# Performance work log

Hardware: AMD Instinct MI355X
Metric: run time of the kernel (lower is better)

Reference implementation:

```python
import jax, jax.numpy as jnp
import numpy as np

E = 1408      # hidden_size
H = 16        # num heads
D = E // H    # head_dim = 88
S = 1025      # (448/14)^2 + 1 cls token
B = 8


def setup_inputs() -> dict:
    key = jax.random.key(0)
    ks = jax.random.split(key, 11)
    scale = 1.0 / np.sqrt(E)
    inp = {
        "hidden_states": jax.random.normal(ks[0], (B, S, E), dtype=jnp.float32),
    }
    # rotary freqs as cos/sin of random angles, shape (S, D//2)
    theta = jax.random.uniform(ks[1], (S, D // 2), dtype=jnp.float32) * (2.0 * np.pi)
    inp["freqs_cos"] = jnp.cos(theta)
    inp["freqs_sin"] = jnp.sin(theta)
    # projection weights stored torch-style: (out_features, in_features)
    inp["q_w"] = jax.random.normal(ks[2], (E, E), dtype=jnp.float32) * scale
    inp["q_b"] = jax.random.normal(ks[3], (E,), dtype=jnp.float32) * scale
    inp["k_w"] = jax.random.normal(ks[4], (E, E), dtype=jnp.float32) * scale
    inp["k_b"] = jax.random.normal(ks[5], (E,), dtype=jnp.float32) * scale
    inp["v_w"] = jax.random.normal(ks[6], (E, E), dtype=jnp.float32) * scale
    inp["v_b"] = jax.random.normal(ks[7], (E,), dtype=jnp.float32) * scale
    inp["o_w"] = jax.random.normal(ks[8], (E, E), dtype=jnp.float32) * scale
    inp["o_b"] = jax.random.normal(ks[9], (E,), dtype=jnp.float32) * scale
    return inp


def _apply_rope(x, cos, sin):
    # x: (B, S, H, D); interpret last dim as D//2 complex pairs (re, im)
    xr = x.astype(jnp.float32).reshape(*x.shape[:-1], D // 2, 2)
    re, im = xr[..., 0], xr[..., 1]
    c = cos[None, :, None, :]  # broadcast over batch and heads
    s = sin[None, :, None, :]
    out_re = re * c - im * s
    out_im = re * s + im * c
    return jnp.stack([out_re, out_im], axis=-1).reshape(x.shape).astype(x.dtype)


def reference(hidden_states, freqs_cos, freqs_sin, q_w, q_b, k_w, k_b, v_w, v_b, o_w, o_b):
    b, s, _ = hidden_states.shape
    q = (hidden_states @ q_w.T + q_b).reshape(b, s, H, D)
    k = (hidden_states @ k_w.T + k_b).reshape(b, s, H, D)
    v = (hidden_states @ v_w.T + v_b).reshape(b, s, H, D)
    q = _apply_rope(q, freqs_cos, freqs_sin)
    k = _apply_rope(k, freqs_cos, freqs_sin)
    # (B, H, S, D)
    q = q.transpose(0, 2, 1, 3)
    k = k.transpose(0, 2, 1, 3)
    v = v.transpose(0, 2, 1, 3)
    scores = jnp.einsum('bhqd,bhkd->bhqk', q, k) / np.sqrt(D)
    attn = jax.nn.softmax(scores.astype(jnp.float32), axis=-1).astype(q.dtype)
    out = jnp.einsum('bhqk,bhkd->bqhd', attn, v).reshape(b, s, H * D)
    out = out @ o_w.T + o_b
    return out, attn
```

## Files before the change

### kernel.cpp

```cpp
#include <hip/hip_runtime.h>

typedef unsigned short u16;
typedef __attribute__((ext_vector_type(8))) short short8;
typedef __attribute__((ext_vector_type(4))) float f32x4;
typedef __attribute__((ext_vector_type(16))) float f32x16;

#define E_DIM 1408
#define H_HEADS 16
#define S_SEQ 1025
#define B_BATCH 8
#define S_PAD 1088
#define D_PAD 128
#define M_ROWS 8200
#define M_PAD 8320

struct __attribute__((packed, aligned(4))) f4u { float x, y, z, w; };

__device__ __forceinline__ u16 f2bf(float f){
  union { float f; unsigned u; } x; x.f = f;
  unsigned r = x.u + 0x7fffu + ((x.u >> 16) & 1u);
  return (u16)(r >> 16);
}

__device__ __forceinline__ void gload16(const void* g, void* l){
  __builtin_amdgcn_global_load_lds(
      (const __attribute__((address_space(1))) void*)g,
      (__attribute__((address_space(3))) void*)l, 16, 0, 0);
}

__device__ __forceinline__ f32x4 mfma16(short8 a, short8 b, f32x4 c){
  return __builtin_amdgcn_mfma_f32_16x16x32_bf16(a, b, c, 0, 0, 0);
}
__device__ __forceinline__ f32x16 mfma32(short8 a, short8 b, f32x16 c){
  return __builtin_amdgcn_mfma_f32_32x32x16_bf16(a, b, c, 0, 0, 0);
}

__device__ __forceinline__ unsigned cvtpk(float a, float b){
  unsigned r;
  asm("v_cvt_pk_bf16_f32 %0, %1, %2" : "=v"(r) : "v"(a), "v"(b));
  return r;
}
__device__ __forceinline__ void plswap(unsigned &a, unsigned &b){
  asm("v_permlane32_swap_b32 %0, %1" : "+v"(a), "+v"(b));
}

__global__ __launch_bounds__(256) void cvt_kernel(const float* __restrict__ src,
                                                  u16* __restrict__ dst, int n8){
  int i = blockIdx.x * 256 + threadIdx.x;
  if (i >= n8) return;
  const float4* s4 = (const float4*)src;
  float4 a = s4[2*i], b = s4[2*i+1];
  union { u16 u[8]; short8 v; } o;
  o.u[0]=f2bf(a.x); o.u[1]=f2bf(a.y); o.u[2]=f2bf(a.z); o.u[3]=f2bf(a.w);
  o.u[4]=f2bf(b.x); o.u[5]=f2bf(b.y); o.u[6]=f2bf(b.z); o.u[7]=f2bf(b.w);
  ((short8*)dst)[i] = o.v;
}

__global__ __launch_bounds__(256) void cvt4_kernel(const float* __restrict__ s0,
                                                   const float* __restrict__ s1,
                                                   const float* __restrict__ s2,
                                                   const float* __restrict__ s3,
                                                   u16* __restrict__ dst, int n8){
  int i = blockIdx.x * 256 + threadIdx.x;
  if (i >= n8) return;
  const float* src = (blockIdx.y == 0) ? s0 : (blockIdx.y == 1) ? s1
                   : (blockIdx.y == 2) ? s2 : s3;
  u16* d = dst + (size_t)blockIdx.y * n8 * 8;
  const float4* s4 = (const float4*)src;
  float4 a = s4[2*i], b = s4[2*i+1];
  union { u16 u[8]; short8 v; } o;
  o.u[0]=f2bf(a.x); o.u[1]=f2bf(a.y); o.u[2]=f2bf(a.z); o.u[3]=f2bf(a.w);
  o.u[4]=f2bf(b.x); o.u[5]=f2bf(b.y); o.u[6]=f2bf(b.z); o.u[7]=f2bf(b.w);
  ((short8*)d)[i] = o.v;
}

__global__ __launch_bounds__(256) void zero_pads_kernel(u16* __restrict__ Q,
                                                        u16* __restrict__ K,
                                                        u16* __restrict__ Vt){
  int i = blockIdx.x * 256 + threadIdx.x;
  const int n1 = 128 * S_PAD * 8;
  const int n2 = 128 * 63 * 96;
  const int n3 = 128 * 96 * 63;
  if (i < n1){
    int d = 88 + (i & 7); int t = i >> 3;
    int s = t % S_PAD; int bh = t / S_PAD;
    size_t o = ((size_t)bh * S_PAD + s) * D_PAD + d;
    Q[o] = 0; K[o] = 0;
  } else if (i < n1 + n2){
    int j = i - n1;
    int d = j % 96; int t = j / 96;
    int s = 1025 + t % 63; int bh = t / 63;
    size_t o = ((size_t)bh * S_PAD + s) * D_PAD + d;
    Q[o] = 0; K[o] = 0;
  } else if (i < n1 + n2 + n3){
    int j = i - n1 - n2;
    int d = j % 96; int t = j / 96;
    int sp = 1025 + t % 63; int bh = t / 63;
    Vt[((size_t)bh * D_PAD + d) * S_PAD + sp] = 0;
  }
}

template<int MODE>
__global__ __launch_bounds__(256) void gemm_bt(
    const u16* __restrict__ A, const u16* __restrict__ W,
    const float* __restrict__ b_q, const float* __restrict__ b_k,
    const float* __restrict__ b_v,
    u16* __restrict__ Qb, u16* __restrict__ Kb, u16* __restrict__ Vtb,
    float* __restrict__ outF,
    const float* __restrict__ fcos, const float* __restrict__ fsin)
{
  __shared__ u16 As[128*32];
  __shared__ u16 Bs[128*32];
  const int tid = threadIdx.x;
  const int lane = tid & 63, wid = tid >> 6;
  const int cl = lane & 15, grp = lane >> 4;

  const int nwg = (int)(gridDim.x * gridDim.y);
  const int orig = blockIdx.x + gridDim.x * blockIdx.y;
  const int qq = nwg >> 3, rr = nwg & 7;
  const int xcd = orig & 7, kk = orig >> 3;
  const int wg = (xcd < rr ? xcd * (qq + 1) : rr * (qq + 1) + (xcd - rr) * qq) + kk;
  const int bx = wg % (int)gridDim.x, by = wg / (int)gridDim.x;

  const int n0 = bx * 128, m0 = by * 128;
  const int region = (MODE == 0) ? (bx / 11) : 0;
  const int wm = (wid >> 1) * 64, wn = (wid & 1) * 64;
  f32x4 acc[4][4] = {};

  for (int k0 = 0; k0 < E_DIM; k0 += 32){
    __syncthreads();
#pragma unroll
    for (int rd = 0; rd < 2; ++rd){
      int G = rd * 256 + tid;
      int row = G >> 2, cg = G & 3;
      gload16(A + (size_t)(m0 + row) * E_DIM + k0 + cg * 8, (char*)As + (size_t)G * 16);
      gload16(W + (size_t)(n0 + row) * E_DIM + k0 + cg * 8, (char*)Bs + (size_t)G * 16);
    }
    __syncthreads();
    short8 av[4], bv[4];
#pragma unroll
    for (int i = 0; i < 4; ++i) av[i] = *(const short8*)&As[(wm + i*16 + cl)*32 + grp*8];
#pragma unroll
    for (int j = 0; j < 4; ++j) bv[j] = *(const short8*)&Bs[(wn + j*16 + cl)*32 + grp*8];
    __builtin_amdgcn_s_setprio(1);
#pragma unroll
    for (int i = 0; i < 4; ++i)
#pragma unroll
      for (int j = 0; j < 4; ++j)
        acc[i][j] = mfma16(av[i], bv[j], acc[i][j]);
    __builtin_amdgcn_s_setprio(0);
  }

  const float* bias = (MODE == 1) ? b_q : (region == 0 ? b_q : (region == 1 ? b_k : b_v));
  const float QSCALE = 0.15379181f;

#pragma unroll
  for (int i = 0; i < 4; ++i){
#pragma unroll
    for (int j = 0; j < 4; ++j){
      const int jcol = n0 + wn + j*16 + cl;
      const int jl = jcol - region * E_DIM;
      const float bsv = bias[jl];
      const int hh = jl / 88;
      const int dd = jl - hh * 88;
#pragma unroll
      for (int r = 0; r < 4; ++r){
        const int rrow = m0 + wm + i*16 + grp*4 + r;
        float v = acc[i][j][r] + bsv;
        if (MODE == 0 && region <= 1){
          float other = __shfl_xor(v, 1);
          int bb = rrow / 1025;
          int spos = rrow - bb * 1025;
          int pp = dd >> 1;
          float c = fcos[spos * 44 + pp];
          float s = fsin[spos * 44 + pp];
          float o = fmaf(v, c, (jl & 1) ? (other * s) : -(other * s));
          if (region == 0) o *= QSCALE;
          if (rrow < M_ROWS){
            size_t dst = (((size_t)(bb * 16 + hh)) * S_PAD + spos) * D_PAD + dd;
            (region ? Kb : Qb)[dst] = f2bf(o);
          }
        } else if (MODE == 0){
          if (rrow < M_ROWS){
            int bb = rrow / 1025;
            int spos = rrow - bb * 1025;
            size_t dst = (((size_t)(bb * 16 + hh)) * D_PAD + dd) * S_PAD + spos;
            Vtb[dst] = f2bf(v);
          }
        } else {
          if (rrow < M_ROWS) outF[(size_t)rrow * E_DIM + jcol] = v;
        }
      }
    }
  }
}

#define STAGE_K(buf, kt)                                                        \
  {                                                                             \
    _Pragma("unroll")                                                           \
    for (int rd = 0; rd < 4; ++rd){                                             \
      int G = rd * 256 + tid;                                                   \
      int row = G >> 4, c = G & 15;                                             \
      gload16(Kg + (size_t)((kt) * 64 + row) * 128 + ((c ^ (row & 15)) * 8),    \
              (char*)&Ks[buf][0] + (size_t)G * 16);                             \
    }                                                                           \
  }

#define STAGE_V(kt)                                                             \
  {                                                                             \
    _Pragma("unroll")                                                           \
    for (int rd = 0; rd < 3; ++rd){                                             \
      int G = rd * 256 + tid;                                                   \
      int row = G >> 3, c = G & 7;                                              \
      gload16(Vg + (size_t)row * S_PAD + (kt) * 64 + ((c ^ (row & 7)) * 8),     \
              (char*)Vs + (size_t)G * 16);                                      \
    }                                                                           \
  }

__global__ __launch_bounds__(256, 3) void attn_kernel(
    const u16* __restrict__ Qb, const u16* __restrict__ Kb,
    const u16* __restrict__ Vtb, float* __restrict__ attn,
    u16* __restrict__ AO)
{
  __shared__ u16 Ks[2][64 * 128];
  __shared__ u16 Vs[96 * 64];
  const int tid = threadIdx.x, wid = tid >> 6, lane = tid & 63;
  const int q5 = lane & 31, hi = lane >> 5;
  int lin = blockIdx.x + gridDim.x * blockIdx.y;
  lin = (lin & 7) * 144 + (lin >> 3);
  const int qt = lin % 9, bh = lin / 9;
  const int b = bh >> 4, h = bh & 15;
  const u16* __restrict__ Qg = Qb + (size_t)bh * S_PAD * 128;
  const u16* __restrict__ Kg = Kb + (size_t)bh * S_PAD * 128;
  const u16* __restrict__ Vg = Vtb + (size_t)bh * 128 * S_PAD;
  const int qrow = qt * 128 + wid * 32 + q5;
  const int qrowc = (qrow < S_PAD) ? qrow : (S_PAD - 1);

  short8 qf[6];
#pragma unroll
  for (int ds = 0; ds < 6; ++ds)
    qf[ds] = *(const short8*)&Qg[(size_t)qrowc * 128 + ds * 16 + hi * 8];

  float l0 = 0.f, l1 = 0.f, l2 = 0.f, l3 = 0.f;
  STAGE_K(0, 0);
  __syncthreads();
  for (int kt = 0; kt < 17; ++kt){
    const int cur = kt & 1;
    if (kt < 16) STAGE_K(cur ^ 1, kt + 1);
#pragma unroll
    for (int ks = 0; ks < 2; ++ks){
      f32x16 sc = {};
      const int krow = ks * 32 + q5;
      __builtin_amdgcn_s_setprio(1);
#pragma unroll
      for (int ds = 0; ds < 6; ++ds){
        int c = ds * 2 + hi;
        short8 kf = *(const short8*)&Ks[cur][krow * 128 + ((c ^ (krow & 15)) * 8)];
        sc = mfma32(kf, qf[ds], sc);
      }
      __builtin_amdgcn_s_setprio(0);
#pragma unroll
      for (int r = 0; r < 16; r += 4){
        l0 += __builtin_amdgcn_exp2f(sc[r]);
        l1 += __builtin_amdgcn_exp2f(sc[r+1]);
        l2 += __builtin_amdgcn_exp2f(sc[r+2]);
        l3 += __builtin_amdgcn_exp2f(sc[r+3]);
      }
    }
    __syncthreads();
  }
  float l = (l0 + l1) + (l2 + l3);
  l += __shfl_xor(l, 32);
  l -= 63.0f;
  const float lg2l = __builtin_amdgcn_logf(l);

  f32x16 oacc[3] = {};
  STAGE_K(0, 0);
  STAGE_V(0);
  __syncthreads();
  for (int kt = 0; kt < 17; ++kt){
    const int cur = kt & 1;
    if (kt < 16) STAGE_K(cur ^ 1, kt + 1);
    short8 pa0[2], pa1[2];
#pragma unroll
    for (int ks = 0; ks < 2; ++ks){
      f32x16 sc = {};
      const int krow = ks * 32 + q5;
      __builtin_amdgcn_s_setprio(1);
#pragma unroll
      for (int ds = 0; ds < 6; ++ds){
        int c = ds * 2 + hi;
        short8 kf = *(const short8*)&Ks[cur][krow * 128 + ((c ^ (krow & 15)) * 8)];
        sc = mfma32(kf, qf[ds], sc);
      }
      __builtin_amdgcn_s_setprio(0);
#pragma unroll
      for (int r = 0; r < 16; ++r) sc[r] = __builtin_amdgcn_exp2f(sc[r] - lg2l);

      if (qrow < 1025){
        if (kt < 16){
          float* arow = attn + ((size_t)bh * 1025 + qrow) * 1025 + kt * 64 + ks * 32 + 4 * hi;
#pragma unroll
          for (int g = 0; g < 4; ++g){
            f4u w4 = { sc[4*g], sc[4*g+1], sc[4*g+2], sc[4*g+3] };
            *(f4u*)(arow + 8 * g) = w4;
          }
        } else {
#pragma unroll
          for (int r = 0; r < 16; ++r){
            int kabs = 1024 + ks * 32 + (r & 3) + 8 * (r >> 2) + 4 * hi;
            if (kabs < 1025)
              attn[((size_t)bh * 1025 + qrow) * 1025 + kabs] = sc[r];
          }
        }
      }

      unsigned w0 = cvtpk(sc[0],  sc[1]),  w1 = cvtpk(sc[2],  sc[3]);
      unsigned w2 = cvtpk(sc[4],  sc[5]),  w3 = cvtpk(sc[6],  sc[7]);
      unsigned w4 = cvtpk(sc[8],  sc[9]),  w5 = cvtpk(sc[10], sc[11]);
      unsigned w6 = cvtpk(sc[12], sc[13]), w7 = cvtpk(sc[14], sc[15]);
      plswap(w0, w2); plswap(w1, w3); plswap(w4, w6); plswap(w5, w7);
      union U { unsigned u[4]; short8 s8; } A0, A1;
      A0.u[0] = w0; A0.u[1] = w1; A0.u[2] = w2; A0.u[3] = w3;
      A1.u[0] = w4; A1.u[1] = w5; A1.u[2] = w6; A1.u[3] = w7;
      pa0[ks] = A0.s8; pa1[ks] = A1.s8;
    }

    __syncthreads();
    __builtin_amdgcn_s_setprio(1);
#pragma unroll
    for (int ks = 0; ks < 2; ++ks){
#pragma unroll
      for (int dt = 0; dt < 3; ++dt){
        const int vrow = dt * 32 + q5;
        int c0 = ks * 4 + hi;
        short8 vf0 = *(const short8*)&Vs[vrow * 64 + ((c0 ^ (vrow & 7)) * 8)];
        oacc[dt] = mfma32(pa0[ks], vf0, oacc[dt]);
        int c1 = ks * 4 + 2 + hi;
        short8 vf1 = *(const short8*)&Vs[vrow * 64 + ((c1 ^ (vrow & 7)) * 8)];
        oacc[dt] = mfma32(pa1[ks], vf1, oacc[dt]);
      }
    }
    __builtin_amdgcn_s_setprio(0);
    __syncthreads();
    if (kt < 16) STAGE_V(kt + 1);
  }

  const int qb0 = qt * 128 + wid * 32;
#pragma unroll
  for (int dt = 0; dt < 3; ++dt){
    const int d = dt * 32 + q5;
    if (d < 88){
#pragma unroll
      for (int r = 0; r < 16; ++r){
        int qq2 = qb0 + (r & 3) + 8 * (r >> 2) + 4 * hi;
        if (qq2 < 1025)
          AO[((size_t)b * 1025 + qq2) * E_DIM + h * 88 + d] = f2bf(oacc[dt][r]);
      }
    }
  }
}

extern "C" void kernel_launch(void* const* d_in, const int* in_sizes, int n_in,
                              void* d_out, int out_size, void* d_ws, size_t ws_size,
                              hipStream_t stream)
{
  const float* hs   = (const float*)d_in[0];
  const float* fcos = (const float*)d_in[1];
  const float* fsin = (const float*)d_in[2];
  const float* q_w  = (const float*)d_in[3];
  const float* q_b  = (const float*)d_in[4];
  const float* k_w  = (const float*)d_in[5];
  const float* k_b  = (const float*)d_in[6];
  const float* v_w  = (const float*)d_in[7];
  const float* v_b  = (const float*)d_in[8];
  const float* o_w  = (const float*)d_in[9];
  const float* o_b  = (const float*)d_in[10];
  float* out0 = (float*)d_out;
  float* attn = out0 + (size_t)B_BATCH * S_SEQ * E_DIM;

  char* ws = (char*)d_ws;
  size_t off = 0;
  auto take = [&](size_t bytes){
    char* p = ws + off; off += (bytes + 255) & ~(size_t)255; return p;
  };
  u16* Xb  = (u16*)take((size_t)M_PAD * E_DIM * 2);
  u16* Wb  = (u16*)take((size_t)4 * E_DIM * E_DIM * 2);
  u16* Qb  = (u16*)take((size_t)128 * S_PAD * D_PAD * 2);
  u16* Kb  = (u16*)take((size_t)128 * S_PAD * D_PAD * 2);
  u16* Vtb = (u16*)take((size_t)128 * D_PAD * S_PAD * 2);
  u16* AO  = (u16*)take((size_t)M_PAD * E_DIM * 2);

  cvt_kernel<<<(1443200 + 255) / 256, 256, 0, stream>>>(hs, Xb, 1443200);
  cvt4_kernel<<<dim3(968, 4), 256, 0, stream>>>(q_w, k_w, v_w, o_w, Wb, 247808);
  zero_pads_kernel<<<10400, 256, 0, stream>>>(Qb, Kb, Vtb);

  gemm_bt<0><<<dim3(33, 65), 256, 0, stream>>>(Xb, Wb, q_b, k_b, v_b,
                                               Qb, Kb, Vtb, nullptr, fcos, fsin);

  attn_kernel<<<dim3(9, 128), 256, 0, stream>>>(Qb, Kb, Vtb, attn, AO);

  gemm_bt<1><<<dim3(11, 65), 256, 0, stream>>>(AO, Wb + 3 * (size_t)E_DIM * E_DIM,
                                               o_b, o_b, o_b,
                                               nullptr, nullptr, nullptr, out0, fcos, fsin);
}
```

Baseline: 547.9 us.

## Use 256x256 double-buffered swizzled tile GEMM for fused QKV projection

Replaces the 128x128 single-buffered QKV GEMM with a 512-thread kernel using 256x256 tiles, K-step 64 split into two halves, double-buffered LDS with async global-to-LDS loads, and an XOR swizzle to cut bank conflicts. Weight buffer is padded to 4352 rows and X to 8448 rows so the larger tiles fit, with masks on the epilogue writes. The output projection moves into its own unchanged-style kernel. The larger tiles and overlapped loads are meant to raise data reuse and hide memory latency. In exchange, LDS and register use per block rise, the padded columns cost wasted MFMA work, and the padded rows/weights are read uninitialized.

```diff
diff --git a/kernel.cpp b/kernel.cpp
--- a/kernel.cpp
+++ b/kernel.cpp
@@ -12,7 +12,9 @@
 #define S_PAD 1088
 #define D_PAD 128
 #define M_ROWS 8200
-#define M_PAD 8320
+#define M_PAD 8448
+#define N_QKV 4224
+#define N_QKV_PAD 4352
 
 struct __attribute__((packed, aligned(4))) f4u { float x, y, z, w; };
 
@@ -56,15 +58,13 @@
   ((short8*)dst)[i] = o.v;
 }
 
-__global__ __launch_bounds__(256) void cvt4_kernel(const float* __restrict__ s0,
+__global__ __launch_bounds__(256) void cvt3_kernel(const float* __restrict__ s0,
                                                    const float* __restrict__ s1,
                                                    const float* __restrict__ s2,
-                                                   const float* __restrict__ s3,
                                                    u16* __restrict__ dst, int n8){
   int i = blockIdx.x * 256 + threadIdx.x;
   if (i >= n8) return;
-  const float* src = (blockIdx.y == 0) ? s0 : (blockIdx.y == 1) ? s1
-                   : (blockIdx.y == 2) ? s2 : s3;
+  const float* src = (blockIdx.y == 0) ? s0 : (blockIdx.y == 1) ? s1 : s2;
   u16* d = dst + (size_t)blockIdx.y * n8 * 8;
   const float4* s4 = (const float4*)src;
   float4 a = s4[2*i], b = s4[2*i+1];
@@ -100,74 +100,105 @@
   }
 }
 
-template<int MODE>
-__global__ __launch_bounds__(256) void gemm_bt(
-    const u16* __restrict__ A, const u16* __restrict__ W,
+#define STG(buf, mat, h, t)                                                     \
+  {                                                                             \
+    const u16* gsrc = (mat) ? (Wq + (size_t)n0 * E_DIM) : (Aq + (size_t)m0 * E_DIM); \
+    _Pragma("unroll")                                                           \
+    for (int rd = 0; rd < 2; ++rd){                                             \
+      int L = rd * 512 + tid;                                                   \
+      int r = L >> 2;                                                           \
+      int g = (L & 3) ^ ((r >> 1) & 3);                                         \
+      gload16(gsrc + (size_t)r * E_DIM + (t) * 64 + (h) * 32 + g * 8,           \
+              (char*)&Ls[buf][mat][h][0] + (size_t)L * 16);                     \
+    }                                                                           \
+  }
+
+#define COMPUTE(buf, ks)                                                        \
+  {                                                                             \
+    short8 av[8], bv[4];                                                        \
+    _Pragma("unroll")                                                           \
+    for (int i = 0; i < 8; ++i){                                                \
+      int R = wm + i * 16 + cl;                                                 \
+      av[i] = *(const short8*)&Ls[buf][0][ks][R * 32 + ((grp ^ ((R >> 1) & 3)) * 8)]; \
+    }                                                                           \
+    _Pragma("unroll")                                                           \
+    for (int j = 0; j < 4; ++j){                                                \
+      int R = wn + j * 16 + cl;                                                 \
+      bv[j] = *(const short8*)&Ls[buf][1][ks][R * 32 + ((grp ^ ((R >> 1) & 3)) * 8)]; \
+    }                                                                           \
+    __builtin_amdgcn_s_setprio(1);                                              \
+    _Pragma("unroll")                                                           \
+    for (int i = 0; i < 8; ++i)                                                 \
+      _Pragma("unroll")                                                         \
+      for (int j = 0; j < 4; ++j)                                               \
+        acc[i][j] = mfma16(av[i], bv[j], acc[i][j]);                            \
+    __builtin_amdgcn_s_setprio(0);                                              \
+  }
+
+#define WAITV(n) asm volatile("s_waitcnt vmcnt(" #n ")" ::: "memory")
+
+__global__ __launch_bounds__(512, 2) void gemm_qkv256(
+    const u16* __restrict__ Aq, const u16* __restrict__ Wq,
     const float* __restrict__ b_q, const float* __restrict__ b_k,
     const float* __restrict__ b_v,
     u16* __restrict__ Qb, u16* __restrict__ Kb, u16* __restrict__ Vtb,
-    float* __restrict__ outF,
     const float* __restrict__ fcos, const float* __restrict__ fsin)
 {
-  __shared__ u16 As[128*32];
-  __shared__ u16 Bs[128*32];
+  __shared__ u16 Ls[2][2][2][256 * 32];
   const int tid = threadIdx.x;
   const int lane = tid & 63, wid = tid >> 6;
   const int cl = lane & 15, grp = lane >> 4;
 
-  const int nwg = (int)(gridDim.x * gridDim.y);
+  const int nwg = 17 * 33;
   const int orig = blockIdx.x + gridDim.x * blockIdx.y;
   const int qq = nwg >> 3, rr = nwg & 7;
   const int xcd = orig & 7, kk = orig >> 3;
   const int wg = (xcd < rr ? xcd * (qq + 1) : rr * (qq + 1) + (xcd - rr) * qq) + kk;
-  const int bx = wg % (int)gridDim.x, by = wg / (int)gridDim.x;
-
-  const int n0 = bx * 128, m0 = by * 128;
-  const int region = (MODE == 0) ? (bx / 11) : 0;
-  const int wm = (wid >> 1) * 64, wn = (wid & 1) * 64;
-  f32x4 acc[4][4] = {};
-
-  for (int k0 = 0; k0 < E_DIM; k0 += 32){
-    __syncthreads();
-#pragma unroll
-    for (int rd = 0; rd < 2; ++rd){
-      int G = rd * 256 + tid;
-      int row = G >> 2, cg = G & 3;
-      gload16(A + (size_t)(m0 + row) * E_DIM + k0 + cg * 8, (char*)As + (size_t)G * 16);
-      gload16(W + (size_t)(n0 + row) * E_DIM + k0 + cg * 8, (char*)Bs + (size_t)G * 16);
-    }
-    __syncthreads();
-    short8 av[4], bv[4];
-#pragma unroll
-    for (int i = 0; i < 4; ++i) av[i] = *(const short8*)&As[(wm + i*16 + cl)*32 + grp*8];
-#pragma unroll
-    for (int j = 0; j < 4; ++j) bv[j] = *(const short8*)&Bs[(wn + j*16 + cl)*32 + grp*8];
-    __builtin_amdgcn_s_setprio(1);
-#pragma unroll
-    for (int i = 0; i < 4; ++i)
-#pragma unroll
-      for (int j = 0; j < 4; ++j)
-        acc[i][j] = mfma16(av[i], bv[j], acc[i][j]);
-    __builtin_amdgcn_s_setprio(0);
-  }
-
-  const float* bias = (MODE == 1) ? b_q : (region == 0 ? b_q : (region == 1 ? b_k : b_v));
+  const int bx = wg % 17, by = wg / 17;
+  const int n0 = bx * 256, m0 = by * 256;
+  const int wm = (wid >> 2) * 128, wn = (wid & 3) * 64;
+
+  f32x4 acc[8][4] = {};
+
+  STG(0, 0, 0, 0); STG(0, 1, 0, 0);
+  STG(0, 0, 1, 0); STG(0, 1, 1, 0);
+
+  for (int kt = 0; kt < 21; ++kt){
+    const int cur = kt & 1, nxt = cur ^ 1;
+    WAITV(4);
+    __builtin_amdgcn_s_barrier();
+    STG(nxt, 0, 0, kt + 1); STG(nxt, 1, 0, kt + 1);
+    COMPUTE(cur, 0);
+    WAITV(4);
+    __builtin_amdgcn_s_barrier();
+    STG(nxt, 0, 1, kt + 1); STG(nxt, 1, 1, kt + 1);
+    COMPUTE(cur, 1);
+  }
+  WAITV(4);
+  __builtin_amdgcn_s_barrier();
+  COMPUTE(1, 0);
+  WAITV(0);
+  __builtin_amdgcn_s_barrier();
+  COMPUTE(1, 1);
+
   const float QSCALE = 0.15379181f;
-
-#pragma unroll
-  for (int i = 0; i < 4; ++i){
-#pragma unroll
-    for (int j = 0; j < 4; ++j){
-      const int jcol = n0 + wn + j*16 + cl;
-      const int jl = jcol - region * E_DIM;
-      const float bsv = bias[jl];
-      const int hh = jl / 88;
-      const int dd = jl - hh * 88;
+#pragma unroll
+  for (int j = 0; j < 4; ++j){
+    const int jcol = n0 + wn + j * 16 + cl;
+    const bool vcol = (jcol < N_QKV);
+    const int region = vcol ? (jcol / E_DIM) : 2;
+    const int jl = jcol - region * E_DIM;
+    const float* bias = (region == 0) ? b_q : (region == 1) ? b_k : b_v;
+    const float bsv = vcol ? bias[jl] : 0.f;
+    const int hh = jl / 88;
+    const int dd = jl - hh * 88;
+#pragma unroll
+    for (int i = 0; i < 8; ++i){
 #pragma unroll
       for (int r = 0; r < 4; ++r){
-        const int rrow = m0 + wm + i*16 + grp*4 + r;
+        const int rrow = m0 + wm + i * 16 + grp * 4 + r;
         float v = acc[i][j][r] + bsv;
-        if (MODE == 0 && region <= 1){
+        if (region <= 1){
           float other = __shfl_xor(v, 1);
           int bb = rrow / 1025;
           int spos = rrow - bb * 1025;
@@ -176,20 +207,78 @@
           float s = fsin[spos * 44 + pp];
           float o = fmaf(v, c, (jl & 1) ? (other * s) : -(other * s));
           if (region == 0) o *= QSCALE;
-          if (rrow < M_ROWS){
+          if (vcol && rrow < M_ROWS && dd < 88){
             size_t dst = (((size_t)(bb * 16 + hh)) * S_PAD + spos) * D_PAD + dd;
             (region ? Kb : Qb)[dst] = f2bf(o);
           }
-        } else if (MODE == 0){
-          if (rrow < M_ROWS){
+        } else {
+          if (vcol && rrow < M_ROWS && dd < 88){
             int bb = rrow / 1025;
             int spos = rrow - bb * 1025;
             size_t dst = (((size_t)(bb * 16 + hh)) * D_PAD + dd) * S_PAD + spos;
             Vtb[dst] = f2bf(v);
           }
-        } else {
-          if (rrow < M_ROWS) outF[(size_t)rrow * E_DIM + jcol] = v;
         }
+      }
+    }
+  }
+}
+
+__global__ __launch_bounds__(256) void gemm_oproj(
+    const u16* __restrict__ A, const u16* __restrict__ W,
+    const float* __restrict__ bias, float* __restrict__ outF)
+{
+  __shared__ u16 As[128*32];
+  __shared__ u16 Bs[128*32];
+  const int tid = threadIdx.x;
+  const int lane = tid & 63, wid = tid >> 6;
+  const int cl = lane & 15, grp = lane >> 4;
+
+  const int nwg = (int)(gridDim.x * gridDim.y);
+  const int orig = blockIdx.x + gridDim.x * blockIdx.y;
+  const int qq = nwg >> 3, rr = nwg & 7;
+  const int xcd = orig & 7, kk = orig >> 3;
+  const int wg = (xcd < rr ? xcd * (qq + 1) : rr * (qq + 1) + (xcd - rr) * qq) + kk;
+  const int bx = wg % (int)gridDim.x, by = wg / (int)gridDim.x;
+
+  const int n0 = bx * 128, m0 = by * 128;
+  const int wm = (wid >> 1) * 64, wn = (wid & 1) * 64;
+  f32x4 acc[4][4] = {};
+
+  for (int k0 = 0; k0 < E_DIM; k0 += 32){
+    __syncthreads();
+#pragma unroll
+    for (int rd = 0; rd < 2; ++rd){
+      int G = rd * 256 + tid;
+      int row = G >> 2, cg = G & 3;
+      gload16(A + (size_t)(m0 + row) * E_DIM + k0 + cg * 8, (char*)As + (size_t)G * 16);
+      gload16(W + (size_t)(n0 + row) * E_DIM + k0 + cg * 8, (char*)Bs + (size_t)G * 16);
+    }
+    __syncthreads();
+    short8 av[4], bv[4];
+#pragma unroll
+    for (int i = 0; i < 4; ++i) av[i] = *(const short8*)&As[(wm + i*16 + cl)*32 + grp*8];
+#pragma unroll
+    for (int j = 0; j < 4; ++j) bv[j] = *(const short8*)&Bs[(wn + j*16 + cl)*32 + grp*8];
+    __builtin_amdgcn_s_setprio(1);
+#pragma unroll
+    for (int i = 0; i < 4; ++i)
+#pragma unroll
+      for (int j = 0; j < 4; ++j)
+        acc[i][j] = mfma16(av[i], bv[j], acc[i][j]);
+    __builtin_amdgcn_s_setprio(0);
+  }
+
+#pragma unroll
+  for (int i = 0; i < 4; ++i){
+#pragma unroll
+    for (int j = 0; j < 4; ++j){
+      const int jcol = n0 + wn + j*16 + cl;
+      const float bsv = bias[jcol];
+#pragma unroll
+      for (int r = 0; r < 4; ++r){
+        const int rrow = m0 + wm + i*16 + grp*4 + r;
+        if (rrow < M_ROWS) outF[(size_t)rrow * E_DIM + jcol] = acc[i][j][r] + bsv;
       }
     }
   }
@@ -384,23 +473,23 @@
   auto take = [&](size_t bytes){
     char* p = ws + off; off += (bytes + 255) & ~(size_t)255; return p;
   };
-  u16* Xb  = (u16*)take((size_t)M_PAD * E_DIM * 2);
-  u16* Wb  = (u16*)take((size_t)4 * E_DIM * E_DIM * 2);
-  u16* Qb  = (u16*)take((size_t)128 * S_PAD * D_PAD * 2);
-  u16* Kb  = (u16*)take((size_t)128 * S_PAD * D_PAD * 2);
-  u16* Vtb = (u16*)take((size_t)128 * D_PAD * S_PAD * 2);
-  u16* AO  = (u16*)take((size_t)M_PAD * E_DIM * 2);
+  u16* Xb   = (u16*)take((size_t)M_PAD * E_DIM * 2);
+  u16* Wqkv = (u16*)take((size_t)N_QKV_PAD * E_DIM * 2);
+  u16* Wo   = (u16*)take((size_t)E_DIM * E_DIM * 2);
+  u16* Qb   = (u16*)take((size_t)128 * S_PAD * D_PAD * 2);
+  u16* Kb   = (u16*)take((size_t)128 * S_PAD * D_PAD * 2);
+  u16* Vtb  = (u16*)take((size_t)128 * D_PAD * S_PAD * 2);
+  u16* AO   = (u16*)take((size_t)M_PAD * E_DIM * 2);
 
   cvt_kernel<<<(1443200 + 255) / 256, 256, 0, stream>>>(hs, Xb, 1443200);
-  cvt4_kernel<<<dim3(968, 4), 256, 0, stream>>>(q_w, k_w, v_w, o_w, Wb, 247808);
+  cvt3_kernel<<<dim3(968, 3), 256, 0, stream>>>(q_w, k_w, v_w, Wqkv, 247808);
+  cvt_kernel<<<968, 256, 0, stream>>>(o_w, Wo, 247808);
   zero_pads_kernel<<<10400, 256, 0, stream>>>(Qb, Kb, Vtb);
 
-  gemm_bt<0><<<dim3(33, 65), 256, 0, stream>>>(Xb, Wb, q_b, k_b, v_b,
-                                               Qb, Kb, Vtb, nullptr, fcos, fsin);
+  gemm_qkv256<<<dim3(17, 33), 512, 0, stream>>>(Xb, Wqkv, q_b, k_b, v_b,
+                                                Qb, Kb, Vtb, fcos, fsin);
 
   attn_kernel<<<dim3(9, 128), 256, 0, stream>>>(Qb, Kb, Vtb, attn, AO);
 
-  gemm_bt<1><<<dim3(11, 65), 256, 0, stream>>>(AO, Wb + 3 * (size_t)E_DIM * E_DIM,
-                                               o_b, o_b, o_b,
-                                               nullptr, nullptr, nullptr, out0, fcos, fsin);
-}
+  gemm_oproj<<<dim3(11, 65), 256, 0, stream>>>(AO, Wo, o_b, out0);
+}
```

Measured after the change: 580.6 us. 1.06x slower.

## Split attention into two kernels and read K/V directly from global memory

Applied to the files above, without the earlier changes.

The fused attention kernel becomes two kernels. The first computes the per-row softmax log-normaliser and stores it to a workspace buffer. The second recomputes the scores, writes the normalised attention and accumulates P·V. Both now load K and V fragments straight from global memory instead of staging them through LDS with barriers, which frees shared memory and removes syncthreads, and pass 1 may run at higher occupancy. The risk is redundant global traffic from uncoalesced, unshared K/V loads, plus an extra launch. Weight conversion is also split into separate QKV and output buffers.

```diff
diff --git a/kernel.cpp b/kernel.cpp
--- a/kernel.cpp
+++ b/kernel.cpp
@@ -13,6 +13,7 @@
 #define D_PAD 128
 #define M_ROWS 8200
 #define M_PAD 8320
+#define N_QKV 4224
 
 struct __attribute__((packed, aligned(4))) f4u { float x, y, z, w; };
 
@@ -56,15 +57,13 @@
   ((short8*)dst)[i] = o.v;
 }
 
-__global__ __launch_bounds__(256) void cvt4_kernel(const float* __restrict__ s0,
+__global__ __launch_bounds__(256) void cvt3_kernel(const float* __restrict__ s0,
                                                    const float* __restrict__ s1,
                                                    const float* __restrict__ s2,
-                                                   const float* __restrict__ s3,
                                                    u16* __restrict__ dst, int n8){
   int i = blockIdx.x * 256 + threadIdx.x;
   if (i >= n8) return;
-  const float* src = (blockIdx.y == 0) ? s0 : (blockIdx.y == 1) ? s1
-                   : (blockIdx.y == 2) ? s2 : s3;
+  const float* src = (blockIdx.y == 0) ? s0 : (blockIdx.y == 1) ? s1 : s2;
   u16* d = dst + (size_t)blockIdx.y * n8 * 8;
   const float4* s4 = (const float4*)src;
   float4 a = s4[2*i], b = s4[2*i+1];
@@ -195,35 +194,61 @@
   }
 }
 
-#define STAGE_K(buf, kt)                                                        \
-  {                                                                             \
-    _Pragma("unroll")                                                           \
-    for (int rd = 0; rd < 4; ++rd){                                             \
-      int G = rd * 256 + tid;                                                   \
-      int row = G >> 4, c = G & 15;                                             \
-      gload16(Kg + (size_t)((kt) * 64 + row) * 128 + ((c ^ (row & 15)) * 8),    \
-              (char*)&Ks[buf][0] + (size_t)G * 16);                             \
-    }                                                                           \
-  }
-
-#define STAGE_V(kt)                                                             \
-  {                                                                             \
-    _Pragma("unroll")                                                           \
-    for (int rd = 0; rd < 3; ++rd){                                             \
-      int G = rd * 256 + tid;                                                   \
-      int row = G >> 3, c = G & 7;                                              \
-      gload16(Vg + (size_t)row * S_PAD + (kt) * 64 + ((c ^ (row & 7)) * 8),     \
-              (char*)Vs + (size_t)G * 16);                                      \
-    }                                                                           \
-  }
-
-__global__ __launch_bounds__(256, 3) void attn_kernel(
+
+__global__ __launch_bounds__(256, 4) void attn_pass1(
     const u16* __restrict__ Qb, const u16* __restrict__ Kb,
-    const u16* __restrict__ Vtb, float* __restrict__ attn,
-    u16* __restrict__ AO)
+    float* __restrict__ lw)
 {
-  __shared__ u16 Ks[2][64 * 128];
-  __shared__ u16 Vs[96 * 64];
+  const int tid = threadIdx.x, wid = tid >> 6, lane = tid & 63;
+  const int q5 = lane & 31, hi = lane >> 5;
+  int lin = blockIdx.x + gridDim.x * blockIdx.y;
+  lin = (lin & 7) * 144 + (lin >> 3);
+  const int qt = lin % 9, bh = lin / 9;
+  const u16* __restrict__ Qg = Qb + (size_t)bh * S_PAD * 128;
+  const u16* __restrict__ Kg = Kb + (size_t)bh * S_PAD * 128;
+  const int qrow = qt * 128 + wid * 32 + q5;
+  const int qrowc = (qrow < S_PAD) ? qrow : (S_PAD - 1);
+
+  short8 qf[6];
+#pragma unroll
+  for (int ds = 0; ds < 6; ++ds)
+    qf[ds] = *(const short8*)&Qg[(size_t)qrowc * 128 + ds * 16 + hi * 8];
+
+  float l0 = 0.f, l1 = 0.f, l2 = 0.f, l3 = 0.f;
+  for (int kt = 0; kt < 17; ++kt){
+#pragma unroll
+    for (int ks = 0; ks < 2; ++ks){
+      const int krow = kt * 64 + ks * 32 + q5;
+      short8 kf[6];
+#pragma unroll
+      for (int ds = 0; ds < 6; ++ds)
+        kf[ds] = *(const short8*)&Kg[(size_t)krow * 128 + (ds * 2 + hi) * 8];
+      f32x16 sc = {};
+      __builtin_amdgcn_s_setprio(1);
+#pragma unroll
+      for (int ds = 0; ds < 6; ++ds) sc = mfma32(kf[ds], qf[ds], sc);
+      __builtin_amdgcn_s_setprio(0);
+#pragma unroll
+      for (int r = 0; r < 16; r += 4){
+        l0 += __builtin_amdgcn_exp2f(sc[r]);
+        l1 += __builtin_amdgcn_exp2f(sc[r+1]);
+        l2 += __builtin_amdgcn_exp2f(sc[r+2]);
+        l3 += __builtin_amdgcn_exp2f(sc[r+3]);
+      }
+    }
+  }
+  float l = (l0 + l1) + (l2 + l3);
+  l += __shfl_xor(l, 32);
+  l -= 63.0f;
+  if (hi == 0 && qrow < S_PAD)
+    lw[(size_t)bh * S_PAD + qrow] = __builtin_amdgcn_logf(l);
+}
+
+__global__ __launch_bounds__(256, 3) void attn_pass2(
+    const u16* __restrict__ Qb, const u16* __restrict__ Kb,
+    const u16* __restrict__ Vtb, const float* __restrict__ lw,
+    float* __restrict__ attn, u16* __restrict__ AO)
+{
   const int tid = threadIdx.x, wid = tid >> 6, lane = tid & 63;
   const int q5 = lane & 31, hi = lane >> 5;
   int lin = blockIdx.x + gridDim.x * blockIdx.y;
@@ -240,62 +265,25 @@
 #pragma unroll
   for (int ds = 0; ds < 6; ++ds)
     qf[ds] = *(const short8*)&Qg[(size_t)qrowc * 128 + ds * 16 + hi * 8];
-
-  float l0 = 0.f, l1 = 0.f, l2 = 0.f, l3 = 0.f;
-  STAGE_K(0, 0);
-  __syncthreads();
+  const float lgl = lw[(size_t)bh * S_PAD + qrowc];
+
+  f32x16 oacc[3] = {};
   for (int kt = 0; kt < 17; ++kt){
-    const int cur = kt & 1;
-    if (kt < 16) STAGE_K(cur ^ 1, kt + 1);
+    short8 pa0[2], pa1[2];
 #pragma unroll
     for (int ks = 0; ks < 2; ++ks){
+      const int krow = kt * 64 + ks * 32 + q5;
+      short8 kf[6];
+#pragma unroll
+      for (int ds = 0; ds < 6; ++ds)
+        kf[ds] = *(const short8*)&Kg[(size_t)krow * 128 + (ds * 2 + hi) * 8];
       f32x16 sc = {};
-      const int krow = ks * 32 + q5;
       __builtin_amdgcn_s_setprio(1);
 #pragma unroll
-      for (int ds = 0; ds < 6; ++ds){
-        int c = ds * 2 + hi;
-        short8 kf = *(const short8*)&Ks[cur][krow * 128 + ((c ^ (krow & 15)) * 8)];
-        sc = mfma32(kf, qf[ds], sc);
-      }
+      for (int ds = 0; ds < 6; ++ds) sc = mfma32(kf[ds], qf[ds], sc);
       __builtin_amdgcn_s_setprio(0);
 #pragma unroll
-      for (int r = 0; r < 16; r += 4){
-        l0 += __builtin_amdgcn_exp2f(sc[r]);
-        l1 += __builtin_amdgcn_exp2f(sc[r+1]);
-        l2 += __builtin_amdgcn_exp2f(sc[r+2]);
-        l3 += __builtin_amdgcn_exp2f(sc[r+3]);
-      }
-    }
-    __syncthreads();
-  }
-  float l = (l0 + l1) + (l2 + l3);
-  l += __shfl_xor(l, 32);
-  l -= 63.0f;
-  const float lg2l = __builtin_amdgcn_logf(l);
-
-  f32x16 oacc[3] = {};
-  STAGE_K(0, 0);
-  STAGE_V(0);
-  __syncthreads();
-  for (int kt = 0; kt < 17; ++kt){
-    const int cur = kt & 1;
-    if (kt < 16) STAGE_K(cur ^ 1, kt + 1);
-    short8 pa0[2], pa1[2];
-#pragma unroll
-    for (int ks = 0; ks < 2; ++ks){
-      f32x16 sc = {};
-      const int krow = ks * 32 + q5;
-      __builtin_amdgcn_s_setprio(1);
-#pragma unroll
-      for (int ds = 0; ds < 6; ++ds){
-        int c = ds * 2 + hi;
-        short8 kf = *(const short8*)&Ks[cur][krow * 128 + ((c ^ (krow & 15)) * 8)];
-        sc = mfma32(kf, qf[ds], sc);
-      }
-      __builtin_amdgcn_s_setprio(0);
-#pragma unroll
-      for (int r = 0; r < 16; ++r) sc[r] = __builtin_amdgcn_exp2f(sc[r] - lg2l);
+      for (int r = 0; r < 16; ++r) sc[r] = __builtin_amdgcn_exp2f(sc[r] - lgl);
 
       if (qrow < 1025){
         if (kt < 16){
@@ -326,24 +314,19 @@
       pa0[ks] = A0.s8; pa1[ks] = A1.s8;
     }
 
-    __syncthreads();
     __builtin_amdgcn_s_setprio(1);
 #pragma unroll
     for (int ks = 0; ks < 2; ++ks){
 #pragma unroll
       for (int dt = 0; dt < 3; ++dt){
         const int vrow = dt * 32 + q5;
-        int c0 = ks * 4 + hi;
-        short8 vf0 = *(const short8*)&Vs[vrow * 64 + ((c0 ^ (vrow & 7)) * 8)];
+        short8 vf0 = *(const short8*)&Vg[(size_t)vrow * S_PAD + kt * 64 + (ks * 4 + hi) * 8];
         oacc[dt] = mfma32(pa0[ks], vf0, oacc[dt]);
-        int c1 = ks * 4 + 2 + hi;
-        short8 vf1 = *(const short8*)&Vs[vrow * 64 + ((c1 ^ (vrow & 7)) * 8)];
+        short8 vf1 = *(const short8*)&Vg[(size_t)vrow * S_PAD + kt * 64 + (ks * 4 + 2 + hi) * 8];
         oacc[dt] = mfma32(pa1[ks], vf1, oacc[dt]);
       }
     }
     __builtin_amdgcn_s_setprio(0);
-    __syncthreads();
-    if (kt < 16) STAGE_V(kt + 1);
   }
 
   const int qb0 = qt * 128 + wid * 32;
@@ -384,23 +367,26 @@
   auto take = [&](size_t bytes){
     char* p = ws + off; off += (bytes + 255) & ~(size_t)255; return p;
   };
-  u16* Xb  = (u16*)take((size_t)M_PAD * E_DIM * 2);
-  u16* Wb  = (u16*)take((size_t)4 * E_DIM * E_DIM * 2);
-  u16* Qb  = (u16*)take((size_t)128 * S_PAD * D_PAD * 2);
-  u16* Kb  = (u16*)take((size_t)128 * S_PAD * D_PAD * 2);
-  u16* Vtb = (u16*)take((size_t)128 * D_PAD * S_PAD * 2);
-  u16* AO  = (u16*)take((size_t)M_PAD * E_DIM * 2);
+  u16* Xb   = (u16*)take((size_t)M_PAD * E_DIM * 2);
+  u16* Wqkv = (u16*)take((size_t)N_QKV * E_DIM * 2);
+  u16* Wo   = (u16*)take((size_t)E_DIM * E_DIM * 2);
+  u16* Qb   = (u16*)take((size_t)128 * S_PAD * D_PAD * 2);
+  u16* Kb   = (u16*)take((size_t)128 * S_PAD * D_PAD * 2);
+  u16* Vtb  = (u16*)take((size_t)128 * D_PAD * S_PAD * 2);
+  u16* AO   = (u16*)take((size_t)M_PAD * E_DIM * 2);
+  float* lw = (float*)take((size_t)128 * S_PAD * 4);
 
   cvt_kernel<<<(1443200 + 255) / 256, 256, 0, stream>>>(hs, Xb, 1443200);
-  cvt4_kernel<<<dim3(968, 4), 256, 0, stream>>>(q_w, k_w, v_w, o_w, Wb, 247808);
+  cvt3_kernel<<<dim3(968, 3), 256, 0, stream>>>(q_w, k_w, v_w, Wqkv, 247808);
+  cvt_kernel<<<968, 256, 0, stream>>>(o_w, Wo, 247808);
   zero_pads_kernel<<<10400, 256, 0, stream>>>(Qb, Kb, Vtb);
 
-  gemm_bt<0><<<dim3(33, 65), 256, 0, stream>>>(Xb, Wb, q_b, k_b, v_b,
+  gemm_bt<0><<<dim3(33, 65), 256, 0, stream>>>(Xb, Wqkv, q_b, k_b, v_b,
                                                Qb, Kb, Vtb, nullptr, fcos, fsin);
 
-  attn_kernel<<<dim3(9, 128), 256, 0, stream>>>(Qb, Kb, Vtb, attn, AO);
-
-  gemm_bt<1><<<dim3(11, 65), 256, 0, stream>>>(AO, Wb + 3 * (size_t)E_DIM * E_DIM,
-                                               o_b, o_b, o_b,
+  attn_pass1<<<dim3(9, 128), 256, 0, stream>>>(Qb, Kb, lw);
+  attn_pass2<<<dim3(9, 128), 256, 0, stream>>>(Qb, Kb, Vtb, lw, attn, AO);
+
+  gemm_bt<1><<<dim3(11, 65), 256, 0, stream>>>(AO, Wo, o_b, o_b, o_b,
                                                nullptr, nullptr, nullptr, out0, fcos, fsin);
 }
```

Result: slower. 766.6 us (+39.9%).

## Transpose attention probabilities through LDS for coalesced stores and stage output epilogue

Applied to the files above, without the earlier changes.

Each wave now writes its bf16-packed probability tile into a per-wave LDS scratch area and reads it back transposed. Consecutive lanes then store consecutive key columns of the large fp32 attention matrix, instead of each lane writing scattered 16-byte chunks of its own row. The attention output epilogue is also staged in LDS so it can go out as 16-byte vector stores. The q/k/v and o weight buffers are split into separate allocations. The trade-offs are extra LDS traffic and occupancy pressure, and the stored attention values are now bf16-rounded rather than full fp32.

```diff
diff --git a/kernel.cpp b/kernel.cpp
--- a/kernel.cpp
+++ b/kernel.cpp
@@ -13,8 +13,7 @@
 #define D_PAD 128
 #define M_ROWS 8200
 #define M_PAD 8320
-
-struct __attribute__((packed, aligned(4))) f4u { float x, y, z, w; };
+#define N_QKV 4224
 
 __device__ __forceinline__ u16 f2bf(float f){
   union { float f; unsigned u; } x; x.f = f;
@@ -56,15 +55,13 @@
   ((short8*)dst)[i] = o.v;
 }
 
-__global__ __launch_bounds__(256) void cvt4_kernel(const float* __restrict__ s0,
+__global__ __launch_bounds__(256) void cvt3_kernel(const float* __restrict__ s0,
                                                    const float* __restrict__ s1,
                                                    const float* __restrict__ s2,
-                                                   const float* __restrict__ s3,
                                                    u16* __restrict__ dst, int n8){
   int i = blockIdx.x * 256 + threadIdx.x;
   if (i >= n8) return;
-  const float* src = (blockIdx.y == 0) ? s0 : (blockIdx.y == 1) ? s1
-                   : (blockIdx.y == 2) ? s2 : s3;
+  const float* src = (blockIdx.y == 0) ? s0 : (blockIdx.y == 1) ? s1 : s2;
   u16* d = dst + (size_t)blockIdx.y * n8 * 8;
   const float4* s4 = (const float4*)src;
   float4 a = s4[2*i], b = s4[2*i+1];
@@ -202,7 +199,7 @@
       int G = rd * 256 + tid;                                                   \
       int row = G >> 4, c = G & 15;                                             \
       gload16(Kg + (size_t)((kt) * 64 + row) * 128 + ((c ^ (row & 15)) * 8),    \
-              (char*)&Ks[buf][0] + (size_t)G * 16);                             \
+              (char*)(KsA + (size_t)(buf) * 8192) + (size_t)G * 16);            \
     }                                                                           \
   }
 
@@ -222,9 +219,11 @@
     const u16* __restrict__ Vtb, float* __restrict__ attn,
     u16* __restrict__ AO)
 {
-  __shared__ u16 Ks[2][64 * 128];
-  __shared__ u16 Vs[96 * 64];
+  __shared__ u16 sm[26624];
   const int tid = threadIdx.x, wid = tid >> 6, lane = tid & 63;
+  u16* const KsA = sm;
+  u16* const Vs  = sm + 16384;
+  u16* const Ps  = sm + 22528 + wid * 1024;
   const int q5 = lane & 31, hi = lane >> 5;
   int lin = blockIdx.x + gridDim.x * blockIdx.y;
   lin = (lin & 7) * 144 + (lin >> 3);
@@ -233,7 +232,8 @@
   const u16* __restrict__ Qg = Qb + (size_t)bh * S_PAD * 128;
   const u16* __restrict__ Kg = Kb + (size_t)bh * S_PAD * 128;
   const u16* __restrict__ Vg = Vtb + (size_t)bh * 128 * S_PAD;
-  const int qrow = qt * 128 + wid * 32 + q5;
+  const int qb0 = qt * 128 + wid * 32;
+  const int qrow = qb0 + q5;
   const int qrowc = (qrow < S_PAD) ? qrow : (S_PAD - 1);
 
   short8 qf[6];
@@ -255,7 +255,7 @@
 #pragma unroll
       for (int ds = 0; ds < 6; ++ds){
         int c = ds * 2 + hi;
-        short8 kf = *(const short8*)&Ks[cur][krow * 128 + ((c ^ (krow & 15)) * 8)];
+        short8 kf = *(const short8*)&KsA[(size_t)cur * 8192 + krow * 128 + ((c ^ (krow & 15)) * 8)];
         sc = mfma32(kf, qf[ds], sc);
       }
       __builtin_amdgcn_s_setprio(0);
@@ -290,30 +290,12 @@
 #pragma unroll
       for (int ds = 0; ds < 6; ++ds){
         int c = ds * 2 + hi;
-        short8 kf = *(const short8*)&Ks[cur][krow * 128 + ((c ^ (krow & 15)) * 8)];
+        short8 kf = *(const short8*)&KsA[(size_t)cur * 8192 + krow * 128 + ((c ^ (krow & 15)) * 8)];
         sc = mfma32(kf, qf[ds], sc);
       }
       __builtin_amdgcn_s_setprio(0);
 #pragma unroll
       for (int r = 0; r < 16; ++r) sc[r] = __builtin_amdgcn_exp2f(sc[r] - lg2l);
-
-      if (qrow < 1025){
-        if (kt < 16){
-          float* arow = attn + ((size_t)bh * 1025 + qrow) * 1025 + kt * 64 + ks * 32 + 4 * hi;
-#pragma unroll
-          for (int g = 0; g < 4; ++g){
-            f4u w4 = { sc[4*g], sc[4*g+1], sc[4*g+2], sc[4*g+3] };
-            *(f4u*)(arow + 8 * g) = w4;
-          }
-        } else {
-#pragma unroll
-          for (int r = 0; r < 16; ++r){
-            int kabs = 1024 + ks * 32 + (r & 3) + 8 * (r >> 2) + 4 * hi;
-            if (kabs < 1025)
-              attn[((size_t)bh * 1025 + qrow) * 1025 + kabs] = sc[r];
-          }
-        }
-      }
 
       unsigned w0 = cvtpk(sc[0],  sc[1]),  w1 = cvtpk(sc[2],  sc[3]);
       unsigned w2 = cvtpk(sc[4],  sc[5]),  w3 = cvtpk(sc[6],  sc[7]);
@@ -324,6 +306,19 @@
       A0.u[0] = w0; A0.u[1] = w1; A0.u[2] = w2; A0.u[3] = w3;
       A1.u[0] = w4; A1.u[1] = w5; A1.u[2] = w6; A1.u[3] = w7;
       pa0[ks] = A0.s8; pa1[ks] = A1.s8;
+
+      *(short8*)&Ps[q5 * 32 + hi * 8]      = pa0[ks];
+      *(short8*)&Ps[q5 * 32 + 16 + hi * 8] = pa1[ks];
+      const int kcol = kt * 64 + ks * 32 + q5;
+      const bool kok = (kt < 16) || (ks == 0 && q5 == 0);
+      float* arow = attn + ((size_t)bh * 1025 + qb0) * 1025 + kcol;
+#pragma unroll
+      for (int p = 0; p < 16; ++p){
+        const int qr2 = qb0 + 2 * p + hi;
+        u16 pv = Ps[(2 * p + hi) * 32 + q5];
+        if (kok && qr2 < 1025)
+          arow[(size_t)(2 * p + hi) * 1025] = __uint_as_float((unsigned)pv << 16);
+      }
     }
 
     __syncthreads();
@@ -346,17 +341,25 @@
     if (kt < 16) STAGE_V(kt + 1);
   }
 
-  const int qb0 = qt * 128 + wid * 32;
+  u16* const Es = sm;
 #pragma unroll
   for (int dt = 0; dt < 3; ++dt){
     const int d = dt * 32 + q5;
-    if (d < 88){
-#pragma unroll
-      for (int r = 0; r < 16; ++r){
-        int qq2 = qb0 + (r & 3) + 8 * (r >> 2) + 4 * hi;
-        if (qq2 < 1025)
-          AO[((size_t)b * 1025 + qq2) * E_DIM + h * 88 + d] = f2bf(oacc[dt][r]);
-      }
+#pragma unroll
+    for (int r = 0; r < 16; ++r){
+      const int ql = wid * 32 + (r & 3) + 8 * (r >> 2) + 4 * hi;
+      Es[ql * 96 + d] = f2bf(oacc[dt][r]);
+    }
+  }
+  __syncthreads();
+  const int qt128 = qt * 128;
+  for (int c = tid; c < 1408; c += 256){
+    const int row = c / 11;
+    const int off = c - row * 11;
+    const int qr = qt128 + row;
+    if (qr < 1025){
+      short8 v = *(const short8*)&Es[row * 96 + off * 8];
+      *(short8*)&AO[((size_t)b * 1025 + qr) * E_DIM + h * 88 + off * 8] = v;
     }
   }
 }
@@ -384,23 +387,24 @@
   auto take = [&](size_t bytes){
     char* p = ws + off; off += (bytes + 255) & ~(size_t)255; return p;
   };
-  u16* Xb  = (u16*)take((size_t)M_PAD * E_DIM * 2);
-  u16* Wb  = (u16*)take((size_t)4 * E_DIM * E_DIM * 2);
-  u16* Qb  = (u16*)take((size_t)128 * S_PAD * D_PAD * 2);
-  u16* Kb  = (u16*)take((size_t)128 * S_PAD * D_PAD * 2);
-  u16* Vtb = (u16*)take((size_t)128 * D_PAD * S_PAD * 2);
-  u16* AO  = (u16*)take((size_t)M_PAD * E_DIM * 2);
+  u16* Xb   = (u16*)take((size_t)M_PAD * E_DIM * 2);
+  u16* Wqkv = (u16*)take((size_t)N_QKV * E_DIM * 2);
+  u16* Wo   = (u16*)take((size_t)E_DIM * E_DIM * 2);
+  u16* Qb   = (u16*)take((size_t)128 * S_PAD * D_PAD * 2);
+  u16* Kb   = (u16*)take((size_t)128 * S_PAD * D_PAD * 2);
+  u16* Vtb  = (u16*)take((size_t)128 * D_PAD * S_PAD * 2);
+  u16* AO   = (u16*)take((size_t)M_PAD * E_DIM * 2);
 
   cvt_kernel<<<(1443200 + 255) / 256, 256, 0, stream>>>(hs, Xb, 1443200);
-  cvt4_kernel<<<dim3(968, 4), 256, 0, stream>>>(q_w, k_w, v_w, o_w, Wb, 247808);
+  cvt3_kernel<<<dim3(968, 3), 256, 0, stream>>>(q_w, k_w, v_w, Wqkv, 247808);
+  cvt_kernel<<<968, 256, 0, stream>>>(o_w, Wo, 247808);
   zero_pads_kernel<<<10400, 256, 0, stream>>>(Qb, Kb, Vtb);
 
-  gemm_bt<0><<<dim3(33, 65), 256, 0, stream>>>(Xb, Wb, q_b, k_b, v_b,
+  gemm_bt<0><<<dim3(33, 65), 256, 0, stream>>>(Xb, Wqkv, q_b, k_b, v_b,
                                                Qb, Kb, Vtb, nullptr, fcos, fsin);
 
   attn_kernel<<<dim3(9, 128), 256, 0, stream>>>(Qb, Kb, Vtb, attn, AO);
 
-  gemm_bt<1><<<dim3(11, 65), 256, 0, stream>>>(AO, Wb + 3 * (size_t)E_DIM * E_DIM,
-                                               o_b, o_b, o_b,
+  gemm_bt<1><<<dim3(11, 65), 256, 0, stream>>>(AO, Wo, o_b, o_b, o_b,
                                                nullptr, nullptr, nullptr, out0, fcos, fsin);
 }
```

Result: slower. 944.7 us (+72.4%).
